# Kernel tuning notes

Measured on AMD Instinct MI355X. Metric: run time of the kernel, lower is better.

Reference implementation:

```python
import jax, jax.numpy as jnp
import numpy as np
import math

D_MODEL = 1024
N_HEADS = 16
D_KV = 64
NUM_BUCKETS = 32
MAX_DISTANCE = 128
BATCH = 4
SEQ = 2048


def _relative_position_bucket(relative_position, num_buckets=NUM_BUCKETS, max_distance=MAX_DISTANCE):
    # bidirectional=True (encoder)
    num_buckets //= 2
    relative_buckets = (relative_position > 0).astype(jnp.int32) * num_buckets
    rp = jnp.abs(relative_position)
    max_exact = num_buckets // 2
    is_small = rp < max_exact
    rp_safe = jnp.maximum(rp, 1)  # avoid log(0); masked by is_small anyway
    rp_if_large = max_exact + (
        jnp.log(rp_safe.astype(jnp.float32) / max_exact)
        / math.log(max_distance / max_exact)
        * (num_buckets - max_exact)
    ).astype(jnp.int32)
    rp_if_large = jnp.minimum(rp_if_large, num_buckets - 1)
    relative_buckets += jnp.where(is_small, rp, rp_if_large)
    return relative_buckets


def compute_bias(rel_bias, q_len, k_len):
    context = jnp.arange(q_len)[:, None]
    memory = jnp.arange(k_len)[None, :]
    buckets = _relative_position_bucket(memory - context)  # [q, k]
    values = rel_bias[buckets]                              # [q, k, h]
    return jnp.transpose(values, (2, 0, 1))[None]           # [1, h, q, k]


def setup_inputs() -> dict:
    key = jax.random.key(0)
    ks = jax.random.split(key, 6)
    s = 1.0 / math.sqrt(D_MODEL)
    return {
        "hidden_states": jax.random.normal(ks[0], (BATCH, SEQ, D_MODEL), jnp.float32),
        "wq": jax.random.normal(ks[1], (D_MODEL, N_HEADS * D_KV), jnp.float32) * s,
        "wk": jax.random.normal(ks[2], (D_MODEL, N_HEADS * D_KV), jnp.float32) * s,
        "wv": jax.random.normal(ks[3], (D_MODEL, N_HEADS * D_KV), jnp.float32) * s,
        "wo": jax.random.normal(ks[4], (N_HEADS * D_KV, D_MODEL), jnp.float32) * s,
        "rel_bias": jax.random.normal(ks[5], (NUM_BUCKETS, N_HEADS), jnp.float32) * 0.5,
    }


def reference(hidden_states, wq, wk, wv, wo, rel_bias):
    B, S, _ = hidden_states.shape

    def shape(x):  # [B,S,H*Dk] -> [B,H,S,Dk]
        return x.reshape(B, S, N_HEADS, D_KV).transpose(0, 2, 1, 3)

    q = shape(hidden_states @ wq)
    k = shape(hidden_states @ wk)
    v = shape(hidden_states @ wv)

    # NOTE: T5 does NOT scale by 1/sqrt(d_kv)
    scores = jnp.einsum("bhqd,bhkd->bhqk", q, k)
    position_bias = compute_bias(rel_bias, S, S)  # [1,H,S,S]
    scores = scores + position_bias
    attn = jax.nn.softmax(scores.astype(jnp.float32), axis=-1).astype(scores.dtype)
    ctx = jnp.einsum("bhqk,bhkd->bhqd", attn, v)
    ctx = ctx.transpose(0, 2, 1, 3).reshape(B, S, N_HEADS * D_KV)
    return ctx @ wo
```

## Files before the change

kernel.cpp:

```cpp
#include <hip/hip_runtime.h>
#include <hip/hip_bf16.h>

typedef unsigned short u16;
typedef unsigned int   u32;
typedef __bf16 bf16x8 __attribute__((ext_vector_type(8)));
typedef __bf16 bf16x4 __attribute__((ext_vector_type(4)));
typedef short  s16x4  __attribute__((ext_vector_type(4)));
typedef float  f32x4  __attribute__((ext_vector_type(4)));
typedef u16    u16x8  __attribute__((ext_vector_type(8)));
typedef u16    u16x4  __attribute__((ext_vector_type(4)));
typedef u32    u32x2  __attribute__((ext_vector_type(2)));

#define MFMA16(a,b,c) __builtin_amdgcn_mfma_f32_16x16x32_bf16(a,b,c,0,0,0)
#define LOG2E 1.4426950408889634f

__device__ __forceinline__ f32x4 mfma16k16(bf16x4 a, bf16x4 b, f32x4 c) {
#if __has_builtin(__builtin_amdgcn_mfma_f32_16x16x16bf16_1k)
    return __builtin_amdgcn_mfma_f32_16x16x16bf16_1k(
        __builtin_bit_cast(s16x4, a), __builtin_bit_cast(s16x4, b), c, 0, 0, 0);
#elif __has_builtin(__builtin_amdgcn_mfma_f32_16x16x16_bf16_1k)
    return __builtin_amdgcn_mfma_f32_16x16x16_bf16_1k(
        __builtin_bit_cast(s16x4, a), __builtin_bit_cast(s16x4, b), c, 0, 0, 0);
#else
    asm("v_mfma_f32_16x16x16_bf16 %0, %1, %2, %0" : "+v"(c) : "v"(a), "v"(b));
    return c;
#endif
}

__device__ __forceinline__ u16 f2b(float f) {
    u32 u = __builtin_bit_cast(u32, f);
    u32 r = (u + 0x7FFFu + ((u >> 16) & 1u)) >> 16;
    return (u16)r;
}

typedef const __attribute__((address_space(1))) u32* gaddr_t;
typedef __attribute__((address_space(3))) u32*       laddr_t;
__device__ __forceinline__ void gl_lds16(const void* g, void* l) {
    __builtin_amdgcn_global_load_lds((gaddr_t)g, (laddr_t)l, 16, 0, 0);
}

__global__ __launch_bounds__(256) void prep_kernel(
        const float* __restrict__ H, const float* __restrict__ wq,
        const float* __restrict__ wk, const float* __restrict__ wv,
        const float* __restrict__ wo, const float* __restrict__ rel_bias,
        u16* __restrict__ Hb, u16* __restrict__ Wt, u16* __restrict__ Wot,
        float* __restrict__ tab) {
    __shared__ u16 tile[64 * 72];
    int bi = blockIdx.x;
    int t = threadIdx.x;
    if (bi < 4096) {
        int i = (bi * 256 + t) * 8;
        float4 a = *(const float4*)(H + i);
        float4 b = *(const float4*)(H + i + 4);
        u16x8 o = { f2b(a.x), f2b(a.y), f2b(a.z), f2b(a.w),
                    f2b(b.x), f2b(b.y), f2b(b.z), f2b(b.w) };
        *(u16x8*)(Hb + i) = o;
    } else if (bi < 5120) {
        int g2 = bi - 4096;
        int g = g2 >> 8, rem = g2 & 255;
        int n0 = (rem >> 4) * 64, k0 = (rem & 15) * 64;
        const float* src = (g == 0) ? wq : (g == 1) ? wk : (g == 2) ? wv : wo;
        u16* dst = (g < 3) ? (Wt + g * 1048576) : Wot;
#pragma unroll
        for (int rr = 0; rr < 4; ++rr) {
            int idx = rr * 256 + t;
            int kr = idx >> 4, c = idx & 15;
            float4 v = *(const float4*)(src + (k0 + kr) * 1024 + n0 + c * 4);
            u16x4 o = { f2b(v.x), f2b(v.y), f2b(v.z), f2b(v.w) };
            *(u16x4*)&tile[kr * 72 + c * 4] = o;
        }
        __syncthreads();
#pragma unroll
        for (int rr = 0; rr < 2; ++rr) {
            int idx = rr * 256 + t;
            int n = idx >> 3, c = idx & 7;
            u16x8 o;
#pragma unroll
            for (int j = 0; j < 8; ++j) o[j] = tile[(c * 8 + j) * 72 + n];
            *(u16x8*)(dst + (n0 + n) * 1024 + k0 + c * 8) = o;
        }
    } else {
        int i = (bi - 5120) * 256 + t;
        int h = i >> 12;
        int idx = i & 4095;
        int delta = idx - 2048;
        int bucket = (delta > 0) ? 16 : 0;
        int rp = delta < 0 ? -delta : delta;
        if (rp < 8) {
            bucket += rp;
        } else {
            float lv = __log2f((float)rp) - 3.0f;
            int tt = (int)(lv * 2.0f);
            int b2 = 8 + tt;
            bucket += (b2 < 15) ? b2 : 15;
        }
        tab[h * 4096 + idx] = rel_bias[bucket * 16 + h] * LOG2E;
    }
}

template <int MODE>
__global__ __launch_bounds__(256) void gemm_bt(
        const u16* __restrict__ A, const u16* __restrict__ Bt, int K, int N,
        u16* __restrict__ q_out, u16* __restrict__ k_out, u16* __restrict__ v_out,
        float* __restrict__ f_out) {
    __shared__ char pool_raw[MODE == 0 ? 128 * 136 * 2 : 32768];
    u16* vt_tile = (u16*)pool_raw;
    int t = threadIdx.x;
    int lane = t & 63, w = t >> 6;
    int wm = w & 1, wn = w >> 1;
    int ln = lane & 15, quad = lane >> 4;
    int bid = (int)blockIdx.x;
    int xcd = bid & 7;
    int r = bid >> 3;
    int by = r >> 3;
    int bxl = r & 7;
    int m0 = (xcd * 8 + bxl) * 128;
    int n0 = by * 128;
    const u16* Ab = A + m0 * K;
    const u16* Bb = Bt + n0 * K;
    f32x4 acc[4][4] = {};
    int nk = K >> 5;

    auto stage = [&](int kt, int buf) {
        int k0 = kt * 32;
        char* Ad = pool_raw + buf * 8192;
        char* Bd = pool_raw + 16384 + buf * 8192;
#pragma unroll
        for (int rr = 0; rr < 2; ++rr) {
            int idx = rr * 256 + t;
            int row = idx >> 2, c = (idx & 3) ^ (row & 3);
            gl_lds16(Ab + row * K + k0 + c * 8, Ad + idx * 16);
            gl_lds16(Bb + row * K + k0 + c * 8, Bd + idx * 16);
        }
    };
    auto compute = [&](int buf) {
        const u16* As = (const u16*)(pool_raw + buf * 8192);
        const u16* Bs = (const u16*)(pool_raw + 16384 + buf * 8192);
        bf16x8 af[4], bfr[4];
#pragma unroll
        for (int mb = 0; mb < 4; ++mb) {
            int row = wm * 64 + mb * 16 + ln;
            af[mb] = *(const bf16x8*)&As[row * 32 + ((quad ^ (row & 3)) << 3)];
        }
#pragma unroll
        for (int nb = 0; nb < 4; ++nb) {
            int row = wn * 64 + nb * 16 + ln;
            bfr[nb] = *(const bf16x8*)&Bs[row * 32 + ((quad ^ (row & 3)) << 3)];
        }
        __builtin_amdgcn_s_setprio(1);
#pragma unroll
        for (int mb = 0; mb < 4; ++mb)
#pragma unroll
            for (int nb = 0; nb < 4; ++nb)
                acc[mb][nb] = MFMA16(af[mb], bfr[nb], acc[mb][nb]);
        __builtin_amdgcn_s_setprio(0);
    };

    stage(0, 0);
    for (int kt = 0; kt < nk - 1; ++kt) {
        stage(kt + 1, (kt + 1) & 1);
        asm volatile("s_waitcnt vmcnt(4)" ::: "memory");
        __builtin_amdgcn_sched_barrier(0);
        __builtin_amdgcn_s_barrier();
        compute(kt & 1);
        __builtin_amdgcn_s_barrier();
    }
    asm volatile("s_waitcnt vmcnt(0)" ::: "memory");
    __builtin_amdgcn_sched_barrier(0);
    __builtin_amdgcn_s_barrier();
    compute((nk - 1) & 1);

    if (MODE == 0 && n0 >= 2048) {
        __syncthreads();
#pragma unroll
        for (int mb = 0; mb < 4; ++mb)
#pragma unroll
            for (int nb = 0; nb < 4; ++nb)
#pragma unroll
                for (int r2 = 0; r2 < 4; ++r2) {
                    int np = wn * 64 + nb * 16 + ln;
                    int mp = wm * 64 + mb * 16 + quad * 4 + r2;
                    vt_tile[np * 136 + mp] = f2b(acc[mb][nb][r2]);
                }
        __syncthreads();
        int h0 = (n0 >> 6) & 15;
        int b = m0 >> 11;
        int s0 = m0 & 2047;
#pragma unroll
        for (int j = 0; j < 8; ++j) {
            int e = j * 256 + t;
            int d_all = e >> 4;
            int sc = e & 15;
            int hh = h0 + (d_all >> 6);
            int d = d_all & 63;
            u16x8 val = *(const u16x8*)&vt_tile[d_all * 136 + sc * 8];
            *(u16x8*)(v_out + (b * 16 + hh) * 131072 + d * 2048 + s0 + sc * 8) = val;
        }
    } else {
#pragma unroll
        for (int mb = 0; mb < 4; ++mb)
#pragma unroll
            for (int nb = 0; nb < 4; ++nb)
#pragma unroll
                for (int r2 = 0; r2 < 4; ++r2) {
                    int m = m0 + wm * 64 + mb * 16 + quad * 4 + r2;
                    int n = n0 + wn * 64 + nb * 16 + ln;
                    float v = acc[mb][nb][r2];
                    if (MODE == 0) {
                        int which = n >> 10, h = (n >> 6) & 15, d = n & 63;
                        int b = m >> 11, s = m & 2047;
                        u16* dst = (which == 0) ? q_out : k_out;
                        float scale = (which == 0) ? LOG2E : 1.0f;
                        dst[(((b << 4) + h) * 2048 + s) * 64 + d] = f2b(v * scale);
                    } else {
                        f_out[m * N + n] = v;
                    }
                }
    }
}

__global__ __launch_bounds__(256, 4) void attn_kernel(
        const u16* __restrict__ Qb, const u16* __restrict__ Kb,
        const u16* __restrict__ Vt, const float* __restrict__ bias_tab,
        u16* __restrict__ ctx) {
    __shared__ u16 Ks[2][64 * 64];
    __shared__ u16 Vs[2][64 * 64];
    __shared__ float sb[384];
    int t = threadIdx.x;
    int lane = t & 63, w = t >> 6;
    int ln = lane & 15, quad = lane >> 4;
    int bid = blockIdx.x;
    int bh = (bid & 7) * 8 + (bid >> 7);
    int qtile = (bid >> 3) & 15;
    int h = bh & 15, b = bh >> 4;
    int q0 = qtile * 128;

    float chi = bias_tab[h * 4096 + 2048 + 1500];
    float clo = bias_tab[h * 4096 + 2048 - 1500];

    const float* tb = bias_tab + h * 4096 + 1857;
    for (int i = t; i < 384; i += 256) sb[i] = tb[i];

    const u16* qbase = Qb + (bh * 2048 + q0 + w * 16 + ln) * 64 + quad * 8;
    bf16x8 qf[2][2];
    qf[0][0] = *(const bf16x8*)(qbase);
    qf[0][1] = *(const bf16x8*)(qbase + 32);
    qf[1][0] = *(const bf16x8*)(qbase + 64 * 64);
    qf[1][1] = *(const bf16x8*)(qbase + 64 * 64 + 32);

    const u16* Kbase = Kb + bh * 2048 * 64;
    const u16* Vbase = Vt + bh * 64 * 2048;

    f32x4 oacc[2][4] = {};
    float l0 = 0.0f, l1 = 0.0f;
    int cb2_base = 191 - w * 16 + quad * 4 - ln;

    auto stage = [&](int kb, int bufidx) {
#pragma unroll
        for (int it = 0; it < 2; ++it) {
            int idx = it * 256 + t;
            int row = idx >> 3, c = (idx & 7) ^ (row & 7);
            gl_lds16(Kbase + (kb + row) * 64 + c * 8,
                     ((char*)&Ks[bufidx][0]) + idx * 16);
            gl_lds16(Vbase + row * 2048 + kb + c * 8,
                     ((char*)&Vs[bufidx][0]) + idx * 16);
        }
    };

    auto compute = [&](int kb0, const u16* Kc, const u16* Vc) {
        f32x4 sacc[2][4];
        int diffs[2] = {kb0 - q0, kb0 - q0 - 64};
        __builtin_amdgcn_s_setprio(1);
#pragma unroll
        for (int nb = 0; nb < 4; ++nb) {
            int key = nb * 16 + ln;
            int sw = key & 7;
            bf16x8 kf0 = *(const bf16x8*)&Kc[key * 64 + ((quad ^ sw) << 3)];
            bf16x8 kf1 = *(const bf16x8*)&Kc[key * 64 + (((quad ^ 4) ^ sw) << 3)];
#pragma unroll
            for (int g = 0; g < 2; ++g) {
                int diff = diffs[g];
                f32x4 ci;
                if (diff >= 192 || diff <= -192) {
                    float c0 = (diff > 0) ? chi : clo;
                    ci = {c0, c0, c0, c0};
                } else {
                    const float* bp = &sb[diff + cb2_base + nb * 16];
                    ci = {bp[0], bp[1], bp[2], bp[3]};
                }
                f32x4 scc = MFMA16(kf0, qf[g][0], ci);
                sacc[g][nb] = MFMA16(kf1, qf[g][1], scc);
            }
        }
        __builtin_amdgcn_s_setprio(0);

        bf16x4 pb[2][4];
#pragma unroll
        for (int g = 0; g < 2; ++g) {
            float s0 = 0.f, s1 = 0.f, s2 = 0.f, s3 = 0.f;
#pragma unroll
            for (int nb = 0; nb < 4; ++nb) {
                float e0 = __builtin_amdgcn_exp2f(sacc[g][nb][0]);
                float e1 = __builtin_amdgcn_exp2f(sacc[g][nb][1]);
                float e2 = __builtin_amdgcn_exp2f(sacc[g][nb][2]);
                float e3 = __builtin_amdgcn_exp2f(sacc[g][nb][3]);
                s0 += e0; s1 += e1; s2 += e2; s3 += e3;
                u32 lo, hi;
                asm("v_cvt_pk_bf16_f32 %0, %1, %2" : "=v"(lo) : "v"(e0), "v"(e1));
                asm("v_cvt_pk_bf16_f32 %0, %1, %2" : "=v"(hi) : "v"(e2), "v"(e3));
                u32x2 uv = {lo, hi};
                pb[g][nb] = __builtin_bit_cast(bf16x4, uv);
            }
            if (g == 0) l0 += (s0 + s1) + (s2 + s3);
            else        l1 += (s0 + s1) + (s2 + s3);
        }

        __builtin_amdgcn_s_setprio(1);
#pragma unroll
        for (int kc = 0; kc < 4; ++kc) {
            bf16x4 vA[4];
#pragma unroll
            for (int nd = 0; nd < 4; ++nd) {
                int d = nd * 16 + ln;
                int ch = (kc * 2 + (quad >> 1)) ^ (d & 7);
                vA[nd] = *(const bf16x4*)&Vc[d * 64 + (ch << 3) + ((quad & 1) << 2)];
            }
#pragma unroll
            for (int nd = 0; nd < 4; ++nd)
#pragma unroll
                for (int g = 0; g < 2; ++g)
                    oacc[g][nd] = mfma16k16(vA[nd], pb[g][kc], oacc[g][nd]);
        }
        __builtin_amdgcn_s_setprio(0);
    };

    stage(0, 0);
    asm volatile("s_waitcnt lgkmcnt(0)" ::: "memory");
    for (int kt = 0; kt < 31; ++kt) {
        int cur = kt & 1;
        stage((kt + 1) * 64, cur ^ 1);
        asm volatile("s_waitcnt vmcnt(4)" ::: "memory");
        __builtin_amdgcn_sched_barrier(0);
        __builtin_amdgcn_s_barrier();
        compute(kt * 64, &Ks[cur][0], &Vs[cur][0]);
        __builtin_amdgcn_s_barrier();
    }
    asm volatile("s_waitcnt vmcnt(0)" ::: "memory");
    __builtin_amdgcn_sched_barrier(0);
    __builtin_amdgcn_s_barrier();
    compute(31 * 64, &Ks[1][0], &Vs[1][0]);

    l0 += __shfl_xor(l0, 16); l0 += __shfl_xor(l0, 32);
    l1 += __shfl_xor(l1, 16); l1 += __shfl_xor(l1, 32);
    float linv[2] = {1.0f / l0, 1.0f / l1};
#pragma unroll
    for (int g = 0; g < 2; ++g) {
        int q = q0 + g * 64 + w * 16 + ln;
        u16* cp = ctx + (b * 2048 + q) * 1024 + h * 64 + quad * 4;
#pragma unroll
        for (int nd = 0; nd < 4; ++nd) {
            u16x4 o = { f2b(oacc[g][nd][0] * linv[g]), f2b(oacc[g][nd][1] * linv[g]),
                        f2b(oacc[g][nd][2] * linv[g]), f2b(oacc[g][nd][3] * linv[g]) };
            *(u16x4*)(cp + nd * 16) = o;
        }
    }
}

extern "C" void kernel_launch(void* const* d_in, const int* in_sizes, int n_in,
                              void* d_out, int out_size, void* d_ws, size_t ws_size,
                              hipStream_t stream) {
    const float* H   = (const float*)d_in[0];
    const float* wq  = (const float*)d_in[1];
    const float* wk  = (const float*)d_in[2];
    const float* wv  = (const float*)d_in[3];
    const float* wo  = (const float*)d_in[4];
    const float* rel = (const float*)d_in[5];
    float* out = (float*)d_out;

    char* ws = (char*)d_ws;
    u16* Hb    = (u16*)(ws);
    u16* Wt    = (u16*)(ws + 16777216);
    u16* Wot   = (u16*)(ws + 23068672);
    u16* Qb    = (u16*)(ws + 25165824);
    u16* Kb    = (u16*)(ws + 41943040);
    u16* Vt    = (u16*)(ws + 58720256);
    float* bias_tab = (float*)(ws + 75497472);
    u16* ctx = Hb;

    prep_kernel<<<5376, 256, 0, stream>>>(H, wq, wk, wv, wo, rel, Hb, Wt, Wot, bias_tab);
    gemm_bt<0><<<1536, 256, 0, stream>>>(Hb, Wt, 1024, 3072, Qb, Kb, Vt, nullptr);
    attn_kernel<<<1024, 256, 0, stream>>>(Qb, Kb, Vt, bias_tab, ctx);
    gemm_bt<1><<<512, 256, 0, stream>>>(ctx, Wot, 1024, 1024, nullptr, nullptr, nullptr, out);
}
```

Before: 272.2 us.

## Double attention query tile to 256 rows per block for K/V reuse

Each attention block now processes 256 query rows (four 64-row groups per wave) instead of 128, halving the grid to 512 blocks. Every K/V tile staged into shared memory is reused across twice as many queries, which halves global K/V traffic and LDS staging per query. K fragments are loaded once per tile and reused across four groups. In exchange, register use roughly doubles (launch bounds lowered to 2 blocks per SIMD), which reduces occupancy and leaves fewer blocks to fill 256 CUs.

```diff
diff --git a/kernel.cpp b/kernel.cpp
--- a/kernel.cpp
+++ b/kernel.cpp
@@ -219,7 +219,7 @@
     }
 }
 
-__global__ __launch_bounds__(256, 4) void attn_kernel(
+__global__ __launch_bounds__(256, 2) void attn_kernel(
         const u16* __restrict__ Qb, const u16* __restrict__ Kb,
         const u16* __restrict__ Vt, const float* __restrict__ bias_tab,
         u16* __restrict__ ctx) {
@@ -230,10 +230,10 @@
     int lane = t & 63, w = t >> 6;
     int ln = lane & 15, quad = lane >> 4;
     int bid = blockIdx.x;
-    int bh = (bid & 7) * 8 + (bid >> 7);
-    int qtile = (bid >> 3) & 15;
+    int bh = (bid & 7) * 8 + (bid >> 6);
+    int qtile = (bid >> 3) & 7;
     int h = bh & 15, b = bh >> 4;
-    int q0 = qtile * 128;
+    int q0 = qtile * 256;
 
     float chi = bias_tab[h * 4096 + 2048 + 1500];
     float clo = bias_tab[h * 4096 + 2048 - 1500];
@@ -242,17 +242,18 @@
     for (int i = t; i < 384; i += 256) sb[i] = tb[i];
 
     const u16* qbase = Qb + (bh * 2048 + q0 + w * 16 + ln) * 64 + quad * 8;
-    bf16x8 qf[2][2];
-    qf[0][0] = *(const bf16x8*)(qbase);
-    qf[0][1] = *(const bf16x8*)(qbase + 32);
-    qf[1][0] = *(const bf16x8*)(qbase + 64 * 64);
-    qf[1][1] = *(const bf16x8*)(qbase + 64 * 64 + 32);
+    bf16x8 qf[4][2];
+#pragma unroll
+    for (int g = 0; g < 4; ++g) {
+        qf[g][0] = *(const bf16x8*)(qbase + g * 4096);
+        qf[g][1] = *(const bf16x8*)(qbase + g * 4096 + 32);
+    }
 
     const u16* Kbase = Kb + bh * 2048 * 64;
     const u16* Vbase = Vt + bh * 64 * 2048;
 
-    f32x4 oacc[2][4] = {};
-    float l0 = 0.0f, l1 = 0.0f;
+    f32x4 oacc[4][4] = {};
+    float lsum[4] = {0.f, 0.f, 0.f, 0.f};
     int cb2_base = 191 - w * 16 + quad * 4 - ln;
 
     auto stage = [&](int kb, int bufidx) {
@@ -268,42 +269,46 @@
     };
 
     auto compute = [&](int kb0, const u16* Kc, const u16* Vc) {
-        f32x4 sacc[2][4];
-        int diffs[2] = {kb0 - q0, kb0 - q0 - 64};
-        __builtin_amdgcn_s_setprio(1);
+        bf16x8 kf[4][2];
 #pragma unroll
         for (int nb = 0; nb < 4; ++nb) {
             int key = nb * 16 + ln;
             int sw = key & 7;
-            bf16x8 kf0 = *(const bf16x8*)&Kc[key * 64 + ((quad ^ sw) << 3)];
-            bf16x8 kf1 = *(const bf16x8*)&Kc[key * 64 + (((quad ^ 4) ^ sw) << 3)];
-#pragma unroll
-            for (int g = 0; g < 2; ++g) {
-                int diff = diffs[g];
-                f32x4 ci;
-                if (diff >= 192 || diff <= -192) {
-                    float c0 = (diff > 0) ? chi : clo;
-                    ci = {c0, c0, c0, c0};
-                } else {
-                    const float* bp = &sb[diff + cb2_base + nb * 16];
-                    ci = {bp[0], bp[1], bp[2], bp[3]};
+            kf[nb][0] = *(const bf16x8*)&Kc[key * 64 + ((quad ^ sw) << 3)];
+            kf[nb][1] = *(const bf16x8*)&Kc[key * 64 + (((quad ^ 4) ^ sw) << 3)];
+        }
+        bf16x4 pb[4][4];
+#pragma unroll
+        for (int g = 0; g < 4; ++g) {
+            int diff = kb0 - q0 - g * 64;
+            f32x4 sg[4];
+            __builtin_amdgcn_s_setprio(1);
+            if (diff >= 192 || diff <= -192) {
+                float c0 = (diff > 0) ? chi : clo;
+                f32x4 ci = {c0, c0, c0, c0};
+#pragma unroll
+                for (int nb = 0; nb < 4; ++nb) {
+                    f32x4 scc = MFMA16(kf[nb][0], qf[g][0], ci);
+                    sg[nb] = MFMA16(kf[nb][1], qf[g][1], scc);
                 }
-                f32x4 scc = MFMA16(kf0, qf[g][0], ci);
-                sacc[g][nb] = MFMA16(kf1, qf[g][1], scc);
+            } else {
+                int cb = diff + cb2_base;
+#pragma unroll
+                for (int nb = 0; nb < 4; ++nb) {
+                    const float* bp = &sb[cb + nb * 16];
+                    f32x4 ci = {bp[0], bp[1], bp[2], bp[3]};
+                    f32x4 scc = MFMA16(kf[nb][0], qf[g][0], ci);
+                    sg[nb] = MFMA16(kf[nb][1], qf[g][1], scc);
+                }
             }
-        }
-        __builtin_amdgcn_s_setprio(0);
-
-        bf16x4 pb[2][4];
-#pragma unroll
-        for (int g = 0; g < 2; ++g) {
+            __builtin_amdgcn_s_setprio(0);
             float s0 = 0.f, s1 = 0.f, s2 = 0.f, s3 = 0.f;
 #pragma unroll
             for (int nb = 0; nb < 4; ++nb) {
-                float e0 = __builtin_amdgcn_exp2f(sacc[g][nb][0]);
-                float e1 = __builtin_amdgcn_exp2f(sacc[g][nb][1]);
-                float e2 = __builtin_amdgcn_exp2f(sacc[g][nb][2]);
-                float e3 = __builtin_amdgcn_exp2f(sacc[g][nb][3]);
+                float e0 = __builtin_amdgcn_exp2f(sg[nb][0]);
+                float e1 = __builtin_amdgcn_exp2f(sg[nb][1]);
+                float e2 = __builtin_amdgcn_exp2f(sg[nb][2]);
+                float e3 = __builtin_amdgcn_exp2f(sg[nb][3]);
                 s0 += e0; s1 += e1; s2 += e2; s3 += e3;
                 u32 lo, hi;
                 asm("v_cvt_pk_bf16_f32 %0, %1, %2" : "=v"(lo) : "v"(e0), "v"(e1));
@@ -311,8 +316,7 @@
                 u32x2 uv = {lo, hi};
                 pb[g][nb] = __builtin_bit_cast(bf16x4, uv);
             }
-            if (g == 0) l0 += (s0 + s1) + (s2 + s3);
-            else        l1 += (s0 + s1) + (s2 + s3);
+            lsum[g] += (s0 + s1) + (s2 + s3);
         }
 
         __builtin_amdgcn_s_setprio(1);
@@ -328,7 +332,7 @@
 #pragma unroll
             for (int nd = 0; nd < 4; ++nd)
 #pragma unroll
-                for (int g = 0; g < 2; ++g)
+                for (int g = 0; g < 4; ++g)
                     oacc[g][nd] = mfma16k16(vA[nd], pb[g][kc], oacc[g][nd]);
         }
         __builtin_amdgcn_s_setprio(0);
@@ -350,17 +354,20 @@
     __builtin_amdgcn_s_barrier();
     compute(31 * 64, &Ks[1][0], &Vs[1][0]);
 
-    l0 += __shfl_xor(l0, 16); l0 += __shfl_xor(l0, 32);
-    l1 += __shfl_xor(l1, 16); l1 += __shfl_xor(l1, 32);
-    float linv[2] = {1.0f / l0, 1.0f / l1};
-#pragma unroll
-    for (int g = 0; g < 2; ++g) {
+#pragma unroll
+    for (int g = 0; g < 4; ++g) {
+        lsum[g] += __shfl_xor(lsum[g], 16);
+        lsum[g] += __shfl_xor(lsum[g], 32);
+    }
+#pragma unroll
+    for (int g = 0; g < 4; ++g) {
+        float linv = 1.0f / lsum[g];
         int q = q0 + g * 64 + w * 16 + ln;
         u16* cp = ctx + (b * 2048 + q) * 1024 + h * 64 + quad * 4;
 #pragma unroll
         for (int nd = 0; nd < 4; ++nd) {
-            u16x4 o = { f2b(oacc[g][nd][0] * linv[g]), f2b(oacc[g][nd][1] * linv[g]),
-                        f2b(oacc[g][nd][2] * linv[g]), f2b(oacc[g][nd][3] * linv[g]) };
+            u16x4 o = { f2b(oacc[g][nd][0] * linv), f2b(oacc[g][nd][1] * linv),
+                        f2b(oacc[g][nd][2] * linv), f2b(oacc[g][nd][3] * linv) };
             *(u16x4*)(cp + nd * 16) = o;
         }
     }
@@ -389,6 +396,6 @@
 
     prep_kernel<<<5376, 256, 0, stream>>>(H, wq, wk, wv, wo, rel, Hb, Wt, Wot, bias_tab);
     gemm_bt<0><<<1536, 256, 0, stream>>>(Hb, Wt, 1024, 3072, Qb, Kb, Vt, nullptr);
-    attn_kernel<<<1024, 256, 0, stream>>>(Qb, Kb, Vt, bias_tab, ctx);
+    attn_kernel<<<512, 256, 0, stream>>>(Qb, Kb, Vt, bias_tab, ctx);
     gemm_bt<1><<<512, 256, 0, stream>>>(ctx, Wot, 1024, 1024, nullptr, nullptr, nullptr, out);
 }
```

Measured after the change: 266.4 us. -2.1%, faster.
